# Optimization experiments

Hardware: AMD Instinct MI355X
Metric: run time of the kernel (lower is better)

## Reference

```python
import jax, jax.numpy as jnp
import numpy as np

B, L, D = 8, 2048, 256
DH = 256.0


def setup_inputs() -> dict:
    key = jax.random.key(0)
    ks = jax.random.split(key, 6)
    s = lambda k, shp: jax.random.normal(k, shp, dtype=jnp.float32)
    return {
        "inputQ": s(ks[0], (B, L, D)),
        "inputK": s(ks[1], (B, L, D)),
        "inputV": s(ks[2], (B, L, D)),
        "Wq": s(ks[3], (D, D)) * 0.05,
        "Wk": s(ks[4], (D, D)) * 0.05,
        "Wv": s(ks[5], (D, D)) * 0.05,
    }


def _skew(qe):
    # qe: [B, L, L] -> pad one zero column at front of last axis,
    # reshape [B, L+1, L], drop first row -> Srel [B, L, L]
    b, l, _ = qe.shape
    cat = jnp.concatenate([jnp.zeros((b, l, 1), qe.dtype), qe], axis=2)  # [B,L,L+1]
    reshaped = cat.reshape(b, l + 1, l)
    return reshaped[:, 1:, :]


def reference(inputQ, inputK, inputV, Wq, Wk, Wv):
    Q = jnp.einsum("bld,de->ble", inputQ, Wq)
    K = jnp.einsum("bld,de->ble", inputK, Wk)
    V = jnp.einsum("bld,de->ble", inputV, Wv)
    E = K - Q                                   # [B,L,D]
    QE = jnp.einsum("bqd,bkd->bqk", Q, E)       # Q @ E^T
    Srel = _skew(QE)
    QKt = jnp.einsum("bqd,bkd->bqk", Q, K)
    attn = jax.nn.softmax((QKt + Srel) / jnp.sqrt(jnp.float32(DH)), axis=-1)
    return jnp.einsum("bqk,bkd->bqd", attn, V)
```

## Files before the change

### kernel.cpp

```cpp
#include <hip/hip_runtime.h>
#include <hip/hip_fp16.h>
#include <stdint.h>

typedef _Float16 f16;
typedef _Float16 f16x2 __attribute__((ext_vector_type(2)));
typedef _Float16 f16x4 __attribute__((ext_vector_type(4)));
typedef _Float16 f16x8 __attribute__((ext_vector_type(8)));
typedef __fp16 fp16x2 __attribute__((ext_vector_type(2)));
typedef float f32x4 __attribute__((ext_vector_type(4)));

#define NB 8
#define NL 2048
#define ND 256
#define QKV_ELEMS (NB * NL * ND)

__device__ __forceinline__ f32x4 mfma16(f16x8 a, f16x8 b, f32x4 c) {
  return __builtin_amdgcn_mfma_f32_16x16x32_f16(a, b, c, 0, 0, 0);
}

__global__ void k0_wt(const float* __restrict__ Wq, const float* __restrict__ Wk,
                      const float* __restrict__ Wv, f16* __restrict__ WT) {
  int id = blockIdx.x * 256 + threadIdx.x;
  int m = id >> 16;
  int r = id & 65535;
  int k = r >> 8, n = r & 255;
  const float* W = (m == 0) ? Wq : (m == 1) ? Wk : Wv;
  WT[m * 65536 + n * 256 + k] = (f16)W[k * 256 + n];
}

__global__ __launch_bounds__(256) void k1_proj(
    const float* __restrict__ Aq, const float* __restrict__ Ak, const float* __restrict__ Av,
    const f16* __restrict__ WT, f16* __restrict__ Qh, f16* __restrict__ Kh,
    f16* __restrict__ Vh) {
  const int m = blockIdx.y;
  const float* A = (m == 0) ? Aq : (m == 1) ? Ak : Av;
  f16* O = (m == 0) ? Qh : (m == 1) ? Kh : Vh;
  const f16* Wm = WT + m * 65536;
  const int row0 = blockIdx.x * 64;
  const int tid = threadIdx.x;
  const int lane = tid & 63, w = tid >> 6;

  __shared__ f16 Ald[64 * 64];
  __shared__ f16 Wld[256 * 64];

  f32x4 acc[16];
#pragma unroll
  for (int i = 0; i < 16; ++i) acc[i] = f32x4{0.f, 0.f, 0.f, 0.f};

  for (int kb = 0; kb < 4; ++kb) {
    __syncthreads();
    {
      const int r = tid >> 2, c0 = (tid & 3) * 16;
      const float* src = A + (size_t)(row0 + r) * ND + kb * 64 + c0;
      f16x8 h0, h1;
#pragma unroll
      for (int j = 0; j < 8; ++j) h0[j] = (f16)src[j];
#pragma unroll
      for (int j = 0; j < 8; ++j) h1[j] = (f16)src[8 + j];
      const int sw = (r & 7) << 4;
      *(f16x8*)((char*)Ald + r * 128 + ((c0 * 2) ^ sw)) = h0;
      *(f16x8*)((char*)Ald + r * 128 + ((c0 * 2 + 16) ^ sw)) = h1;
    }
    {
      const int n = tid;
      const f16* src = Wm + n * 256 + kb * 64;
      const int sw = (n & 7) << 4;
#pragma unroll
      for (int j = 0; j < 8; ++j) {
        f16x8 v = *(const f16x8*)(src + j * 8);
        *(f16x8*)((char*)Wld + n * 128 + ((j * 16) ^ sw)) = v;
      }
    }
    __syncthreads();
#pragma unroll
    for (int kk = 0; kk < 2; ++kk) {
      const int arow = w * 16 + (lane & 15);
      const int ko = kk * 64 + (lane >> 4) * 16;
      f16x8 a = *(const f16x8*)((char*)Ald + arow * 128 + (ko ^ ((arow & 7) << 4)));
#pragma unroll
      for (int nt = 0; nt < 16; ++nt) {
        const int n = nt * 16 + (lane & 15);
        f16x8 b = *(const f16x8*)((char*)Wld + n * 128 + (ko ^ ((n & 7) << 4)));
        acc[nt] = mfma16(a, b, acc[nt]);
      }
    }
  }
  const int rl = (lane >> 4) * 4;
#pragma unroll
  for (int nt = 0; nt < 16; ++nt) {
    const int col = nt * 16 + (lane & 15);
#pragma unroll
    for (int j = 0; j < 4; ++j)
      O[(size_t)(row0 + w * 16 + rl + j) * ND + col] = (f16)acc[nt][j];
  }
}

__global__ __launch_bounds__(256) void k2_qe(const f16* __restrict__ Qh,
                                             const f16* __restrict__ Kh,
                                             f16* __restrict__ QEh) {
  const int b = blockIdx.z;
  const int m0 = blockIdx.x * 128, n0 = blockIdx.y * 128;
  const int tid = threadIdx.x, lane = tid & 63, w = tid >> 6;
  const int wr = (w >> 1) * 64, wc = (w & 1) * 64;
  const f16* Qb = Qh + (size_t)b * NL * ND;
  const f16* Kb = Kh + (size_t)b * NL * ND;

  __shared__ f16 As[128 * 64];
  __shared__ f16 Bs[128 * 64];

  f32x4 acc[4][4];
#pragma unroll
  for (int i = 0; i < 4; ++i)
#pragma unroll
    for (int j = 0; j < 4; ++j) acc[i][j] = f32x4{0.f, 0.f, 0.f, 0.f};

  for (int kb = 0; kb < 4; ++kb) {
    __syncthreads();
#pragma unroll
    for (int j = 0; j < 4; ++j) {
      const int c = j * 256 + tid;
      const int r = c >> 3;
      const int ko = (c & 7) * 16;
      const int sw = (r & 7) << 4;
      f16x8 va = *(const f16x8*)((const char*)(Qb + (size_t)(m0 + r) * ND + kb * 64) + ko);
      *(f16x8*)((char*)As + r * 128 + (ko ^ sw)) = va;
      f16x8 vk = *(const f16x8*)((const char*)(Kb + (size_t)(n0 + r) * ND + kb * 64) + ko);
      f16x8 vq = *(const f16x8*)((const char*)(Qb + (size_t)(n0 + r) * ND + kb * 64) + ko);
      *(f16x8*)((char*)Bs + r * 128 + (ko ^ sw)) = vk - vq;
    }
    __syncthreads();
#pragma unroll
    for (int kk = 0; kk < 2; ++kk) {
      const int ko = kk * 64 + (lane >> 4) * 16;
      f16x8 a[4], bf[4];
#pragma unroll
      for (int mt = 0; mt < 4; ++mt) {
        const int r = wr + mt * 16 + (lane & 15);
        a[mt] = *(const f16x8*)((char*)As + r * 128 + (ko ^ ((r & 7) << 4)));
      }
#pragma unroll
      for (int nt = 0; nt < 4; ++nt) {
        const int r = wc + nt * 16 + (lane & 15);
        bf[nt] = *(const f16x8*)((char*)Bs + r * 128 + (ko ^ ((r & 7) << 4)));
      }
#pragma unroll
      for (int mt = 0; mt < 4; ++mt)
#pragma unroll
        for (int nt = 0; nt < 4; ++nt) acc[mt][nt] = mfma16(a[mt], bf[nt], acc[mt][nt]);
    }
  }
  f16* outb = QEh + (size_t)b * NL * NL;
#pragma unroll
  for (int mt = 0; mt < 4; ++mt)
#pragma unroll
    for (int nt = 0; nt < 4; ++nt) {
      const int col = n0 + wc + nt * 16 + (lane & 15);
#pragma unroll
      for (int j = 0; j < 4; ++j) {
        const int row = m0 + wr + mt * 16 + (lane >> 4) * 4 + j;
        outb[(size_t)row * NL + col] = (f16)acc[mt][nt][j];
      }
    }
}

#define KVBUF 36864
#define NITP 16
__global__ __launch_bounds__(256, 2) void k3_part(
    const f16* __restrict__ Qh, const f16* __restrict__ Kh, const f16* __restrict__ Vh,
    const f16* __restrict__ QEh, f16* __restrict__ Pac, float* __restrict__ Pml) {
  __shared__ char smem[KVBUF];
  const int b = blockIdx.y;
  const int g = blockIdx.z;
  const int q0 = blockIdx.x * 64;
  const int tid = threadIdx.x, lane = tid & 63, w = tid >> 6;
  const int qw = q0 + w * 16;
  const int gi = lane >> 4;

  const f16* Qb = Qh + (size_t)b * NL * ND;
  const f16* Kb = Kh + (size_t)b * NL * ND;
  const f16* Vb = Vh + (size_t)b * NL * ND;
  const f16* QEb = QEh + (size_t)b * NL * NL;

  f16x8 qf[8];
  {
    const int r = qw + (lane & 15);
#pragma unroll
    for (int kk = 0; kk < 8; ++kk)
      qf[kk] = *(const f16x8*)(Qb + (size_t)r * ND + kk * 32 + gi * 8);
  }

  f32x4 acc[16];
#pragma unroll
  for (int i = 0; i < 16; ++i) acc[i] = f32x4{0.f, 0.f, 0.f, 0.f};
  float mrun = -1e30f, lrun = 0.f;

  f16x8 kst[4], vst[4];
  const int kp = tid & 15, dch = tid >> 4;

  auto stage_load = [&](int t) {
    const f16* Ks = Kb + (size_t)(g * NITP + t) * 32 * ND;
#pragma unroll
    for (int j = 0; j < 4; ++j) {
      const int c = j * 256 + tid;
      kst[j] = *(const f16x8*)(Ks + (c >> 5) * ND + (c & 31) * 8);
    }
    const f16* Vs = Vb + (size_t)(g * NITP + t) * 32 * ND;
    vst[0] = *(const f16x8*)(Vs + (2 * kp) * ND + dch * 16);
    vst[1] = *(const f16x8*)(Vs + (2 * kp) * ND + dch * 16 + 8);
    vst[2] = *(const f16x8*)(Vs + (2 * kp + 1) * ND + dch * 16);
    vst[3] = *(const f16x8*)(Vs + (2 * kp + 1) * ND + dch * 16 + 8);
  };
  auto stage_write = [&]() {
    char* Kld = smem;
    char* Vld = smem + 16384;
#pragma unroll
    for (int j = 0; j < 4; ++j) {
      const int c = j * 256 + tid;
      const int key = c >> 5, d0 = (c & 31) * 16;
      *(f16x8*)(Kld + key * 512 + (d0 ^ ((key & 7) << 4))) = kst[j];
    }
#pragma unroll
    for (int jj = 0; jj < 16; ++jj) {
      f16x2 pr;
      pr.x = (jj < 8) ? vst[0][jj & 7] : vst[1][jj & 7];
      pr.y = (jj < 8) ? vst[2][jj & 7] : vst[3][jj & 7];
      *(f16x2*)(Vld + (dch * 16 + jj) * 80 + kp * 4) = pr;
    }
  };

  stage_load(0);
  stage_write();
  __syncthreads();

  const int qa = qw + (lane & 15);

  for (int t = 0; t < NITP; ++t) {
    const int k0 = (g * NITP + t) * 32;

    float srel[2][4];
#pragma unroll
    for (int nt = 0; nt < 2; ++nt)
#pragma unroll
      for (int j = 0; j < 4; ++j) {
        const int k = k0 + nt * 16 + gi * 4 + j;
        const int dq = k - qa;
        const size_t a1 = (size_t)qa * NL + (size_t)(NL - 1 + dq);
        const size_t a2 = (size_t)(qa + 1) * NL + (size_t)(dq - 2);
        const float v = (float)QEb[(dq <= 0) ? a1 : a2];
        srel[nt][j] = (dq == 1) ? 0.f : v;
      }

    if (t < NITP - 1) stage_load(t + 1);

    const char* Kld = smem;
    const char* Vld = smem + 16384;

    f32x4 s[2] = {f32x4{0.f, 0.f, 0.f, 0.f}, f32x4{0.f, 0.f, 0.f, 0.f}};
#pragma unroll
    for (int kk = 0; kk < 8; ++kk) {
      const int ko = kk * 64 + gi * 16;
#pragma unroll
      for (int nt = 0; nt < 2; ++nt) {
        const int key = nt * 16 + (lane & 15);
        f16x8 af = *(const f16x8*)(Kld + key * 512 + (ko ^ ((key & 7) << 4)));
        s[nt] = mfma16(af, qf[kk], s[nt]);
      }
    }

    float sv[2][4];
#pragma unroll
    for (int nt = 0; nt < 2; ++nt)
#pragma unroll
      for (int j = 0; j < 4; ++j) sv[nt][j] = 0.0625f * (s[nt][j] + srel[nt][j]);

    float pm = fmaxf(fmaxf(fmaxf(sv[0][0], sv[0][1]), fmaxf(sv[0][2], sv[0][3])),
                     fmaxf(fmaxf(sv[1][0], sv[1][1]), fmaxf(sv[1][2], sv[1][3])));
    pm = fmaxf(pm, __shfl_xor(pm, 16, 64));
    pm = fmaxf(pm, __shfl_xor(pm, 32, 64));

    float p[2][4];
    if (__any(pm > mrun + 8.f)) {
      const float mn = fmaxf(mrun, pm);
      const float al = __expf(mrun - mn);
      mrun = mn;
#pragma unroll
      for (int nt = 0; nt < 2; ++nt)
#pragma unroll
        for (int j = 0; j < 4; ++j) p[nt][j] = __expf(sv[nt][j] - mrun);
      float rs = (p[0][0] + p[0][1]) + (p[0][2] + p[0][3]) +
                 (p[1][0] + p[1][1]) + (p[1][2] + p[1][3]);
      rs += __shfl_xor(rs, 16, 64);
      rs += __shfl_xor(rs, 32, 64);
      lrun = lrun * al + rs;
#pragma unroll
      for (int j = 0; j < 4; ++j) {
        const float aj = __shfl(al, gi * 4 + j, 16);
#pragma unroll
        for (int dt = 0; dt < 16; ++dt) acc[dt][j] *= aj;
      }
    } else {
#pragma unroll
      for (int nt = 0; nt < 2; ++nt)
#pragma unroll
        for (int j = 0; j < 4; ++j) p[nt][j] = __expf(sv[nt][j] - mrun);
      float rs = (p[0][0] + p[0][1]) + (p[0][2] + p[0][3]) +
                 (p[1][0] + p[1][1]) + (p[1][2] + p[1][3]);
      rs += __shfl_xor(rs, 16, 64);
      rs += __shfl_xor(rs, 32, 64);
      lrun += rs;
    }

    union {
      fp16x2 h2[2];
      f16x4 h4;
    } pu0, pu1;
    pu0.h2[0] = __builtin_amdgcn_cvt_pkrtz(p[0][0], p[0][1]);
    pu0.h2[1] = __builtin_amdgcn_cvt_pkrtz(p[0][2], p[0][3]);
    pu1.h2[0] = __builtin_amdgcn_cvt_pkrtz(p[1][0], p[1][1]);
    pu1.h2[1] = __builtin_amdgcn_cvt_pkrtz(p[1][2], p[1][3]);

#pragma unroll
    for (int dt = 0; dt < 16; ++dt) {
      const char* vrow = Vld + (dt * 16 + (lane & 15)) * 80 + 8 * gi;
      f16x4 v0 = *(const f16x4*)(vrow);
      f16x4 v1 = *(const f16x4*)(vrow + 32);
      acc[dt] = __builtin_amdgcn_mfma_f32_16x16x16f16(pu0.h4, v0, acc[dt], 0, 0, 0);
      acc[dt] = __builtin_amdgcn_mfma_f32_16x16x16f16(pu1.h4, v1, acc[dt], 0, 0, 0);
    }

    __syncthreads();
    if (t < NITP - 1) stage_write();
    __syncthreads();
  }

  const float inv = 1.f / lrun;
  f16* Pb = Pac + ((size_t)g * (NB * NL) + (size_t)b * NL) * ND;
#pragma unroll
  for (int j = 0; j < 4; ++j) {
    const float invj = __shfl(inv, gi * 4 + j, 16);
    const int row = qw + gi * 4 + j;
#pragma unroll
    for (int dt = 0; dt < 16; ++dt)
      Pb[(size_t)row * ND + dt * 16 + (lane & 15)] = (f16)(acc[dt][j] * invj);
  }
  if (lane < 16) {
    const size_t r = (size_t)g * (NB * NL) + (size_t)b * NL + qw + lane;
    Pml[r * 2 + 0] = mrun;
    Pml[r * 2 + 1] = lrun;
  }
}

__global__ __launch_bounds__(256) void k4_comb(const f16* __restrict__ Pac,
                                               const float* __restrict__ Pml,
                                               float* __restrict__ Out) {
  const int row = blockIdx.x * 4 + (threadIdx.x >> 6);
  const int lane = threadIdx.x & 63;
  float m[4], l[4];
#pragma unroll
  for (int gq = 0; gq < 4; ++gq) {
    const size_t r = (size_t)gq * (NB * NL) + row;
    m[gq] = Pml[r * 2 + 0];
    l[gq] = Pml[r * 2 + 1];
  }
  const float M = fmaxf(fmaxf(m[0], m[1]), fmaxf(m[2], m[3]));
  float wgt[4];
  float denom = 0.f;
#pragma unroll
  for (int gq = 0; gq < 4; ++gq) {
    wgt[gq] = l[gq] * __expf(m[gq] - M);
    denom += wgt[gq];
  }
  const float inv = 1.f / denom;
  const size_t base = (size_t)row * ND + lane * 4;
  float o[4] = {0.f, 0.f, 0.f, 0.f};
#pragma unroll
  for (int gq = 0; gq < 4; ++gq) {
    f16x4 p = *(const f16x4*)(Pac + (size_t)gq * (NB * NL) * ND + base);
    const float s = wgt[gq] * inv;
#pragma unroll
    for (int e = 0; e < 4; ++e) o[e] += (float)p[e] * s;
  }
  f32x4 ov = {o[0], o[1], o[2], o[3]};
  *(f32x4*)(Out + base) = ov;
}

#define NIT 32
__global__ __launch_bounds__(512, 2) void k3_attn(
    const f16* __restrict__ Qh, const f16* __restrict__ Kh, const f16* __restrict__ Vh,
    const f16* __restrict__ QEh, float* __restrict__ Out) {
  extern __shared__ char smemd[];
  const int b = blockIdx.y;
  const int q0 = blockIdx.x * 64;
  const int tid = threadIdx.x, lane = tid & 63, w = tid >> 6;
  const int g = w >> 2, wq = w & 3;
  const int qw = q0 + wq * 16;
  const int lt = tid & 255;
  const int gi = lane >> 4;

  float* Cst = (float*)smemd;
  float* ml = (float*)(smemd + 65536);

  const f16* Qb = Qh + (size_t)b * NL * ND;
  const f16* Kb = Kh + (size_t)b * NL * ND;
  const f16* Vb = Vh + (size_t)b * NL * ND;
  const f16* QEb = QEh + (size_t)b * NL * NL;

  f16x8 qf[8];
  {
    const int r = qw + (lane & 15);
#pragma unroll
    for (int kk = 0; kk < 8; ++kk)
      qf[kk] = *(const f16x8*)(Qb + (size_t)r * ND + kk * 32 + gi * 8);
  }

  f32x4 acc[16];
#pragma unroll
  for (int i = 0; i < 16; ++i) acc[i] = f32x4{0.f, 0.f, 0.f, 0.f};
  float mrun = -1e30f, lrun = 0.f;

  f16x8 kst[4], vst[4];
  const int kp = lt & 15, dch = lt >> 4;

  auto stage_load = [&](int t) {
    const f16* Ks = Kb + (size_t)(g * NIT + t) * 32 * ND;
#pragma unroll
    for (int j = 0; j < 4; ++j) {
      const int c = j * 256 + lt;
      kst[j] = *(const f16x8*)(Ks + (c >> 5) * ND + (c & 31) * 8);
    }
    const f16* Vs = Vb + (size_t)(g * NIT + t) * 32 * ND;
    vst[0] = *(const f16x8*)(Vs + (2 * kp) * ND + dch * 16);
    vst[1] = *(const f16x8*)(Vs + (2 * kp) * ND + dch * 16 + 8);
    vst[2] = *(const f16x8*)(Vs + (2 * kp + 1) * ND + dch * 16);
    vst[3] = *(const f16x8*)(Vs + (2 * kp + 1) * ND + dch * 16 + 8);
  };
  auto stage_write = [&]() {
    char* Kld = smemd + g * KVBUF;
    char* Vld = Kld + 16384;
#pragma unroll
    for (int j = 0; j < 4; ++j) {
      const int c = j * 256 + lt;
      const int key = c >> 5, d0 = (c & 31) * 16;
      *(f16x8*)(Kld + key * 512 + (d0 ^ ((key & 7) << 4))) = kst[j];
    }
#pragma unroll
    for (int jj = 0; jj < 16; ++jj) {
      f16x2 pr;
      pr.x = (jj < 8) ? vst[0][jj & 7] : vst[1][jj & 7];
      pr.y = (jj < 8) ? vst[2][jj & 7] : vst[3][jj & 7];
      *(f16x2*)(Vld + (dch * 16 + jj) * 80 + kp * 4) = pr;
    }
  };

  stage_load(0);
  stage_write();
  __syncthreads();

  const int qa = qw + (lane & 15);

  for (int t = 0; t < NIT; ++t) {
    const int k0 = (g * NIT + t) * 32;

    float srel[2][4];
#pragma unroll
    for (int nt = 0; nt < 2; ++nt)
#pragma unroll
      for (int j = 0; j < 4; ++j) {
        const int k = k0 + nt * 16 + gi * 4 + j;
        const int dq = k - qa;
        const size_t a1 = (size_t)qa * NL + (size_t)(NL - 1 + dq);
        const size_t a2 = (size_t)(qa + 1) * NL + (size_t)(dq - 2);
        const float v = (float)QEb[(dq <= 0) ? a1 : a2];
        srel[nt][j] = (dq == 1) ? 0.f : v;
      }

    if (t < NIT - 1) stage_load(t + 1);

    const char* Kld = smemd + g * KVBUF;
    const char* Vld = Kld + 16384;

    f32x4 s[2] = {f32x4{0.f, 0.f, 0.f, 0.f}, f32x4{0.f, 0.f, 0.f, 0.f}};
#pragma unroll
    for (int kk = 0; kk < 8; ++kk) {
      const int ko = kk * 64 + gi * 16;
#pragma unroll
      for (int nt = 0; nt < 2; ++nt) {
        const int key = nt * 16 + (lane & 15);
        f16x8 af = *(const f16x8*)(Kld + key * 512 + (ko ^ ((key & 7) << 4)));
        s[nt] = mfma16(af, qf[kk], s[nt]);
      }
    }

    float sv[2][4];
#pragma unroll
    for (int nt = 0; nt < 2; ++nt)
#pragma unroll
      for (int j = 0; j < 4; ++j) sv[nt][j] = 0.0625f * (s[nt][j] + srel[nt][j]);

    float pm = fmaxf(fmaxf(fmaxf(sv[0][0], sv[0][1]), fmaxf(sv[0][2], sv[0][3])),
                     fmaxf(fmaxf(sv[1][0], sv[1][1]), fmaxf(sv[1][2], sv[1][3])));
    pm = fmaxf(pm, __shfl_xor(pm, 16, 64));
    pm = fmaxf(pm, __shfl_xor(pm, 32, 64));

    float p[2][4];
    if (__any(pm > mrun + 8.f)) {
      const float mn = fmaxf(mrun, pm);
      const float al = __expf(mrun - mn);
      mrun = mn;
#pragma unroll
      for (int nt = 0; nt < 2; ++nt)
#pragma unroll
        for (int j = 0; j < 4; ++j) p[nt][j] = __expf(sv[nt][j] - mrun);
      float rs = (p[0][0] + p[0][1]) + (p[0][2] + p[0][3]) +
                 (p[1][0] + p[1][1]) + (p[1][2] + p[1][3]);
      rs += __shfl_xor(rs, 16, 64);
      rs += __shfl_xor(rs, 32, 64);
      lrun = lrun * al + rs;
#pragma unroll
      for (int j = 0; j < 4; ++j) {
        const float aj = __shfl(al, gi * 4 + j, 16);
#pragma unroll
        for (int dt = 0; dt < 16; ++dt) acc[dt][j] *= aj;
      }
    } else {
#pragma unroll
      for (int nt = 0; nt < 2; ++nt)
#pragma unroll
        for (int j = 0; j < 4; ++j) p[nt][j] = __expf(sv[nt][j] - mrun);
      float rs = (p[0][0] + p[0][1]) + (p[0][2] + p[0][3]) +
                 (p[1][0] + p[1][1]) + (p[1][2] + p[1][3]);
      rs += __shfl_xor(rs, 16, 64);
      rs += __shfl_xor(rs, 32, 64);
      lrun += rs;
    }

    union {
      fp16x2 h2[2];
      f16x4 h4;
    } pu0, pu1;
    pu0.h2[0] = __builtin_amdgcn_cvt_pkrtz(p[0][0], p[0][1]);
    pu0.h2[1] = __builtin_amdgcn_cvt_pkrtz(p[0][2], p[0][3]);
    pu1.h2[0] = __builtin_amdgcn_cvt_pkrtz(p[1][0], p[1][1]);
    pu1.h2[1] = __builtin_amdgcn_cvt_pkrtz(p[1][2], p[1][3]);

#pragma unroll
    for (int dt = 0; dt < 16; ++dt) {
      const char* vrow = Vld + (dt * 16 + (lane & 15)) * 80 + 8 * gi;
      f16x4 v0 = *(const f16x4*)(vrow);
      f16x4 v1 = *(const f16x4*)(vrow + 32);
      acc[dt] = __builtin_amdgcn_mfma_f32_16x16x16f16(pu0.h4, v0, acc[dt], 0, 0, 0);
      acc[dt] = __builtin_amdgcn_mfma_f32_16x16x16f16(pu1.h4, v1, acc[dt], 0, 0, 0);
    }

    __syncthreads();
    if (t < NIT - 1) stage_write();
    __syncthreads();
  }

  if (g == 1) {
#pragma unroll
    for (int dt = 0; dt < 16; ++dt)
#pragma unroll
      for (int j = 0; j < 4; ++j)
        Cst[wq * 4096 + (gi * 4 + j) * 256 + dt * 16 + (lane & 15)] = acc[dt][j];
    if (lane < 16) {
      ml[(wq * 16 + lane) * 2 + 0] = mrun;
      ml[(wq * 16 + lane) * 2 + 1] = lrun;
    }
  }
  __syncthreads();
  if (g == 0) {
    float* Ob = Out + (size_t)b * NL * ND;
#pragma unroll
    for (int j = 0; j < 4; ++j) {
      const int rloc = gi * 4 + j;
      const float m0r = __shfl(mrun, rloc, 16);
      const float l0r = __shfl(lrun, rloc, 16);
      const float m1 = ml[(wq * 16 + rloc) * 2 + 0];
      const float l1 = ml[(wq * 16 + rloc) * 2 + 1];
      const float M = fmaxf(m0r, m1);
      const float c0 = __expf(m0r - M), c1 = __expf(m1 - M);
      const float inv = 1.f / (l0r * c0 + l1 * c1);
      const int row = qw + rloc;
#pragma unroll
      for (int dt = 0; dt < 16; ++dt) {
        const float o1 = Cst[wq * 4096 + rloc * 256 + dt * 16 + (lane & 15)];
        Ob[(size_t)row * ND + dt * 16 + (lane & 15)] = (acc[dt][j] * c0 + o1 * c1) * inv;
      }
    }
  }
}

extern "C" void kernel_launch(void* const* d_in, const int* in_sizes, int n_in,
                              void* d_out, int out_size, void* d_ws, size_t ws_size,
                              hipStream_t stream) {
  (void)in_sizes; (void)n_in; (void)out_size;
  const float* inQ = (const float*)d_in[0];
  const float* inK = (const float*)d_in[1];
  const float* inV = (const float*)d_in[2];
  const float* Wq = (const float*)d_in[3];
  const float* Wk = (const float*)d_in[4];
  const float* Wv = (const float*)d_in[5];
  float* out = (float*)d_out;

  f16* ws = (f16*)d_ws;
  f16* Qh = ws;
  f16* Kh = Qh + (size_t)QKV_ELEMS;
  f16* Vh = Kh + (size_t)QKV_ELEMS;
  f16* WT = Vh + (size_t)QKV_ELEMS;
  f16* QEh = WT + 3 * 65536;
  f16* Pac = QEh + (size_t)NB * NL * NL;
  float* Pml = (float*)(Pac + (size_t)4 * QKV_ELEMS);
  const size_t need = (size_t)((char*)(Pml + 4 * NB * NL * 2) - (char*)d_ws);

  k0_wt<<<dim3(768), dim3(256), 0, stream>>>(Wq, Wk, Wv, WT);
  k1_proj<<<dim3(256, 3), dim3(256), 0, stream>>>(inQ, inK, inV, WT, Qh, Kh, Vh);
  k2_qe<<<dim3(16, 16, 8), dim3(256), 0, stream>>>(Qh, Kh, QEh);
  if (ws_size >= need) {
    k3_part<<<dim3(32, 8, 4), dim3(256), 0, stream>>>(Qh, Kh, Vh, QEh, Pac, Pml);
    k4_comb<<<dim3(NB * NL / 4), dim3(256), 0, stream>>>(Pac, Pml, out);
  } else {
    k3_attn<<<dim3(32, 8), dim3(512), 73728, stream>>>(Qh, Kh, Vh, QEh, out);
  }
}
```

Before: 189.9 us.

## Split PV by head-dim across waves, pretranspose V, async-copy K to LDS

Adds a kernel that transposes V into a d-major layout so each wave loads its own V fragments straight from global memory. The P@V work is repartitioned: each wave covers a 64-wide slice of the head dimension for all 64 queries, with P tiles and rescale factors exchanged through shared memory. K tiles are double-buffered in LDS with global_load_lds, which removes the register staging and one barrier per iteration. The cost is an extra transpose pass, more workspace, and LDS traffic for sharing P, and the new path runs only when the workspace is large enough.

```diff
diff --git a/kernel.cpp b/kernel.cpp
--- a/kernel.cpp
+++ b/kernel.cpp
@@ -16,6 +16,12 @@
 
 __device__ __forceinline__ f32x4 mfma16(f16x8 a, f16x8 b, f32x4 c) {
   return __builtin_amdgcn_mfma_f32_16x16x32_f16(a, b, c, 0, 0, 0);
+}
+
+__device__ __forceinline__ void gl_lds16(const void* g, void* l) {
+  __builtin_amdgcn_global_load_lds(
+      (const __attribute__((address_space(1))) void*)g,
+      (__attribute__((address_space(3))) void*)l, 16, 0, 0);
 }
 
 __global__ void k0_wt(const float* __restrict__ Wq, const float* __restrict__ Wk,
@@ -95,6 +101,33 @@
   }
 }
 
+__global__ __launch_bounds__(256) void k1c_vt(const f16* __restrict__ Vh,
+                                              f16* __restrict__ VT) {
+  const int b = blockIdx.z;
+  const int k0 = blockIdx.x * 64;
+  const int d0 = blockIdx.y * 64;
+  __shared__ f16 T[64][72];
+  const int tid = threadIdx.x;
+  const f16* Vb = Vh + (size_t)b * NL * ND;
+  {
+    const int r = tid >> 2, c = (tid & 3) * 16;
+    f16x8 a = *(const f16x8*)(Vb + (size_t)(k0 + r) * ND + d0 + c);
+    f16x8 bq = *(const f16x8*)(Vb + (size_t)(k0 + r) * ND + d0 + c + 8);
+    *(f16x8*)&T[r][c] = a;
+    *(f16x8*)&T[r][c + 8] = bq;
+  }
+  __syncthreads();
+  {
+    const int d = tid >> 2, c = (tid & 3) * 16;
+    f16 tmp[16];
+#pragma unroll
+    for (int j = 0; j < 16; ++j) tmp[j] = T[c + j][d];
+    f16* dst = VT + (size_t)b * ND * NL + (size_t)(d0 + d) * NL + k0 + c;
+    *(f16x8*)dst = *(f16x8*)&tmp[0];
+    *(f16x8*)(dst + 8) = *(f16x8*)&tmp[8];
+  }
+}
+
 __global__ __launch_bounds__(256) void k2_qe(const f16* __restrict__ Qh,
                                              const f16* __restrict__ Kh,
                                              f16* __restrict__ QEh) {
@@ -163,78 +196,55 @@
     }
 }
 
-#define KVBUF 36864
 #define NITP 16
 __global__ __launch_bounds__(256, 2) void k3_part(
-    const f16* __restrict__ Qh, const f16* __restrict__ Kh, const f16* __restrict__ Vh,
+    const f16* __restrict__ Qh, const f16* __restrict__ Kh, const f16* __restrict__ VT,
     const f16* __restrict__ QEh, f16* __restrict__ Pac, float* __restrict__ Pml) {
-  __shared__ char smem[KVBUF];
-  const int b = blockIdx.y;
-  const int g = blockIdx.z;
-  const int q0 = blockIdx.x * 64;
-  const int tid = threadIdx.x, lane = tid & 63, w = tid >> 6;
+  __shared__ char Kld[2][16384];
+  __shared__ char Pfr[2][4096];
+  __shared__ float alf[2][64];
+  __shared__ int rfl[2][4];
+  __shared__ float mlinv[64];
+
+  const int b = blockIdx.y, g = blockIdx.z, q0 = blockIdx.x * 64;
+  const int tid = threadIdx.x, lane = tid & 63, w = tid >> 6, gi = lane >> 4;
   const int qw = q0 + w * 16;
-  const int gi = lane >> 4;
+  const int dbase = w * 64;
 
   const f16* Qb = Qh + (size_t)b * NL * ND;
   const f16* Kb = Kh + (size_t)b * NL * ND;
-  const f16* Vb = Vh + (size_t)b * NL * ND;
+  const f16* VTb = VT + (size_t)b * ND * NL;
   const f16* QEb = QEh + (size_t)b * NL * NL;
 
+  const int qa = qw + (lane & 15);
   f16x8 qf[8];
-  {
-    const int r = qw + (lane & 15);
-#pragma unroll
-    for (int kk = 0; kk < 8; ++kk)
-      qf[kk] = *(const f16x8*)(Qb + (size_t)r * ND + kk * 32 + gi * 8);
-  }
-
-  f32x4 acc[16];
-#pragma unroll
-  for (int i = 0; i < 16; ++i) acc[i] = f32x4{0.f, 0.f, 0.f, 0.f};
+#pragma unroll
+  for (int kk = 0; kk < 8; ++kk)
+    qf[kk] = *(const f16x8*)(Qb + (size_t)qa * ND + kk * 32 + gi * 8);
+
+  f32x4 acc[4][4];
+#pragma unroll
+  for (int i = 0; i < 4; ++i)
+#pragma unroll
+    for (int j = 0; j < 4; ++j) acc[i][j] = f32x4{0.f, 0.f, 0.f, 0.f};
   float mrun = -1e30f, lrun = 0.f;
 
-  f16x8 kst[4], vst[4];
-  const int kp = tid & 15, dch = tid >> 4;
-
-  auto stage_load = [&](int t) {
-    const f16* Ks = Kb + (size_t)(g * NITP + t) * 32 * ND;
-#pragma unroll
-    for (int j = 0; j < 4; ++j) {
-      const int c = j * 256 + tid;
-      kst[j] = *(const f16x8*)(Ks + (c >> 5) * ND + (c & 31) * 8);
-    }
-    const f16* Vs = Vb + (size_t)(g * NITP + t) * 32 * ND;
-    vst[0] = *(const f16x8*)(Vs + (2 * kp) * ND + dch * 16);
-    vst[1] = *(const f16x8*)(Vs + (2 * kp) * ND + dch * 16 + 8);
-    vst[2] = *(const f16x8*)(Vs + (2 * kp + 1) * ND + dch * 16);
-    vst[3] = *(const f16x8*)(Vs + (2 * kp + 1) * ND + dch * 16 + 8);
+  auto kstage = [&](int t, int buf) {
+    const char* src = (const char*)(Kb + (size_t)(g * NITP + t) * 32 * ND);
+#pragma unroll
+    for (int i = 0; i < 4; ++i) {
+      const int chunk = w * 4 + i;
+      const int r = chunk * 2 + (lane >> 5);
+      const int co = ((lane & 31) * 16) ^ ((r & 7) << 4);
+      gl_lds16(src + r * 512 + co, Kld[buf] + chunk * 1024);
+    }
   };
-  auto stage_write = [&]() {
-    char* Kld = smem;
-    char* Vld = smem + 16384;
-#pragma unroll
-    for (int j = 0; j < 4; ++j) {
-      const int c = j * 256 + tid;
-      const int key = c >> 5, d0 = (c & 31) * 16;
-      *(f16x8*)(Kld + key * 512 + (d0 ^ ((key & 7) << 4))) = kst[j];
-    }
-#pragma unroll
-    for (int jj = 0; jj < 16; ++jj) {
-      f16x2 pr;
-      pr.x = (jj < 8) ? vst[0][jj & 7] : vst[1][jj & 7];
-      pr.y = (jj < 8) ? vst[2][jj & 7] : vst[3][jj & 7];
-      *(f16x2*)(Vld + (dch * 16 + jj) * 80 + kp * 4) = pr;
-    }
-  };
-
-  stage_load(0);
-  stage_write();
+
+  kstage(0, 0);
   __syncthreads();
 
-  const int qa = qw + (lane & 15);
-
   for (int t = 0; t < NITP; ++t) {
+    const int pb = t & 1;
     const int k0 = (g * NITP + t) * 32;
 
     float srel[2][4];
@@ -250,10 +260,7 @@
         srel[nt][j] = (dq == 1) ? 0.f : v;
       }
 
-    if (t < NITP - 1) stage_load(t + 1);
-
-    const char* Kld = smem;
-    const char* Vld = smem + 16384;
+    if (t < NITP - 1) kstage(t + 1, pb ^ 1);
 
     f32x4 s[2] = {f32x4{0.f, 0.f, 0.f, 0.f}, f32x4{0.f, 0.f, 0.f, 0.f}};
 #pragma unroll
@@ -262,7 +269,7 @@
 #pragma unroll
       for (int nt = 0; nt < 2; ++nt) {
         const int key = nt * 16 + (lane & 15);
-        f16x8 af = *(const f16x8*)(Kld + key * 512 + (ko ^ ((key & 7) << 4)));
+        f16x8 af = *(const f16x8*)(Kld[pb] + key * 512 + (ko ^ ((key & 7) << 4)));
         s[nt] = mfma16(af, qf[kk], s[nt]);
       }
     }
@@ -278,37 +285,26 @@
     pm = fmaxf(pm, __shfl_xor(pm, 16, 64));
     pm = fmaxf(pm, __shfl_xor(pm, 32, 64));
 
+    const int doresc = (int)__any(pm > mrun + 8.f);
+    if (lane == 0) rfl[pb][w] = doresc;
+
     float p[2][4];
-    if (__any(pm > mrun + 8.f)) {
+    float al = 1.f;
+    if (doresc) {
       const float mn = fmaxf(mrun, pm);
-      const float al = __expf(mrun - mn);
+      al = __expf(mrun - mn);
       mrun = mn;
-#pragma unroll
-      for (int nt = 0; nt < 2; ++nt)
-#pragma unroll
-        for (int j = 0; j < 4; ++j) p[nt][j] = __expf(sv[nt][j] - mrun);
-      float rs = (p[0][0] + p[0][1]) + (p[0][2] + p[0][3]) +
-                 (p[1][0] + p[1][1]) + (p[1][2] + p[1][3]);
-      rs += __shfl_xor(rs, 16, 64);
-      rs += __shfl_xor(rs, 32, 64);
-      lrun = lrun * al + rs;
-#pragma unroll
-      for (int j = 0; j < 4; ++j) {
-        const float aj = __shfl(al, gi * 4 + j, 16);
-#pragma unroll
-        for (int dt = 0; dt < 16; ++dt) acc[dt][j] *= aj;
-      }
-    } else {
-#pragma unroll
-      for (int nt = 0; nt < 2; ++nt)
-#pragma unroll
-        for (int j = 0; j < 4; ++j) p[nt][j] = __expf(sv[nt][j] - mrun);
-      float rs = (p[0][0] + p[0][1]) + (p[0][2] + p[0][3]) +
-                 (p[1][0] + p[1][1]) + (p[1][2] + p[1][3]);
-      rs += __shfl_xor(rs, 16, 64);
-      rs += __shfl_xor(rs, 32, 64);
-      lrun += rs;
-    }
+    }
+#pragma unroll
+    for (int nt = 0; nt < 2; ++nt)
+#pragma unroll
+      for (int j = 0; j < 4; ++j) p[nt][j] = __expf(sv[nt][j] - mrun);
+    float rs = (p[0][0] + p[0][1]) + (p[0][2] + p[0][3]) +
+               (p[1][0] + p[1][1]) + (p[1][2] + p[1][3]);
+    rs += __shfl_xor(rs, 16, 64);
+    rs += __shfl_xor(rs, 32, 64);
+    lrun = lrun * al + rs;
+    if (gi == 0) alf[pb][w * 16 + (lane & 15)] = al;
 
     union {
       fp16x2 h2[2];
@@ -318,36 +314,60 @@
     pu0.h2[1] = __builtin_amdgcn_cvt_pkrtz(p[0][2], p[0][3]);
     pu1.h2[0] = __builtin_amdgcn_cvt_pkrtz(p[1][0], p[1][1]);
     pu1.h2[1] = __builtin_amdgcn_cvt_pkrtz(p[1][2], p[1][3]);
-
-#pragma unroll
-    for (int dt = 0; dt < 16; ++dt) {
-      const char* vrow = Vld + (dt * 16 + (lane & 15)) * 80 + 8 * gi;
-      f16x4 v0 = *(const f16x4*)(vrow);
-      f16x4 v1 = *(const f16x4*)(vrow + 32);
-      acc[dt] = __builtin_amdgcn_mfma_f32_16x16x16f16(pu0.h4, v0, acc[dt], 0, 0, 0);
-      acc[dt] = __builtin_amdgcn_mfma_f32_16x16x16f16(pu1.h4, v1, acc[dt], 0, 0, 0);
-    }
+    *(f16x4*)(Pfr[pb] + (w * 2 + 0) * 512 + lane * 8) = pu0.h4;
+    *(f16x4*)(Pfr[pb] + (w * 2 + 1) * 512 + lane * 8) = pu1.h4;
+
+    f16x4 vf[4][2];
+#pragma unroll
+    for (int dt = 0; dt < 4; ++dt)
+#pragma unroll
+      for (int nt = 0; nt < 2; ++nt)
+        vf[dt][nt] = *(const f16x4*)(VTb + (size_t)(dbase + dt * 16 + (lane & 15)) * NL +
+                                     k0 + nt * 16 + 4 * gi);
 
     __syncthreads();
-    if (t < NITP - 1) stage_write();
-    __syncthreads();
-  }
-
-  const float inv = 1.f / lrun;
-  f16* Pb = Pac + ((size_t)g * (NB * NL) + (size_t)b * NL) * ND;
-#pragma unroll
-  for (int j = 0; j < 4; ++j) {
-    const float invj = __shfl(inv, gi * 4 + j, 16);
-    const int row = qw + gi * 4 + j;
-#pragma unroll
-    for (int dt = 0; dt < 16; ++dt)
-      Pb[(size_t)row * ND + dt * 16 + (lane & 15)] = (f16)(acc[dt][j] * invj);
-  }
+
+    if (rfl[pb][0] | rfl[pb][1] | rfl[pb][2] | rfl[pb][3]) {
+#pragma unroll
+      for (int qt = 0; qt < 4; ++qt)
+#pragma unroll
+        for (int j = 0; j < 4; ++j) {
+          const float a = alf[pb][qt * 16 + 4 * gi + j];
+#pragma unroll
+          for (int dt = 0; dt < 4; ++dt) acc[qt][dt][j] *= a;
+        }
+    }
+
+#pragma unroll
+    for (int qt = 0; qt < 4; ++qt) {
+      f16x4 pa0 = *(const f16x4*)(Pfr[pb] + (qt * 2 + 0) * 512 + lane * 8);
+      f16x4 pa1 = *(const f16x4*)(Pfr[pb] + (qt * 2 + 1) * 512 + lane * 8);
+#pragma unroll
+      for (int dt = 0; dt < 4; ++dt) {
+        acc[qt][dt] = __builtin_amdgcn_mfma_f32_16x16x16f16(pa0, vf[dt][0], acc[qt][dt], 0, 0, 0);
+        acc[qt][dt] = __builtin_amdgcn_mfma_f32_16x16x16f16(pa1, vf[dt][1], acc[qt][dt], 0, 0, 0);
+      }
+    }
+  }
+
+  if (gi == 0) mlinv[w * 16 + (lane & 15)] = 1.f / lrun;
   if (lane < 16) {
     const size_t r = (size_t)g * (NB * NL) + (size_t)b * NL + qw + lane;
     Pml[r * 2 + 0] = mrun;
     Pml[r * 2 + 1] = lrun;
   }
+  __syncthreads();
+  f16* Pb = Pac + ((size_t)g * (NB * NL) + (size_t)b * NL + q0) * ND;
+#pragma unroll
+  for (int qt = 0; qt < 4; ++qt)
+#pragma unroll
+    for (int j = 0; j < 4; ++j) {
+      const int row = qt * 16 + 4 * gi + j;
+      const float iv = mlinv[row];
+#pragma unroll
+      for (int dt = 0; dt < 4; ++dt)
+        Pb[(size_t)row * ND + dbase + dt * 16 + (lane & 15)] = (f16)(acc[qt][dt][j] * iv);
+    }
 }
 
 __global__ __launch_bounds__(256) void k4_comb(const f16* __restrict__ Pac,
@@ -384,6 +404,7 @@
   *(f32x4*)(Out + base) = ov;
 }
 
+#define KVBUF 36864
 #define NIT 32
 __global__ __launch_bounds__(512, 2) void k3_attn(
     const f16* __restrict__ Qh, const f16* __restrict__ Kh, const f16* __restrict__ Vh,
@@ -611,13 +632,15 @@
   f16* QEh = WT + 3 * 65536;
   f16* Pac = QEh + (size_t)NB * NL * NL;
   float* Pml = (float*)(Pac + (size_t)4 * QKV_ELEMS);
-  const size_t need = (size_t)((char*)(Pml + 4 * NB * NL * 2) - (char*)d_ws);
+  f16* VT = (f16*)(Pml + 4 * NB * NL * 2);
+  const size_t need = (size_t)((char*)(VT + (size_t)QKV_ELEMS) - (char*)d_ws);
 
   k0_wt<<<dim3(768), dim3(256), 0, stream>>>(Wq, Wk, Wv, WT);
   k1_proj<<<dim3(256, 3), dim3(256), 0, stream>>>(inQ, inK, inV, WT, Qh, Kh, Vh);
   k2_qe<<<dim3(16, 16, 8), dim3(256), 0, stream>>>(Qh, Kh, QEh);
   if (ws_size >= need) {
-    k3_part<<<dim3(32, 8, 4), dim3(256), 0, stream>>>(Qh, Kh, Vh, QEh, Pac, Pml);
+    k1c_vt<<<dim3(32, 4, 8), dim3(256), 0, stream>>>(Vh, VT);
+    k3_part<<<dim3(32, 8, 4), dim3(256), 0, stream>>>(Qh, Kh, VT, QEh, Pac, Pml);
     k4_comb<<<dim3(NB * NL / 4), dim3(256), 0, stream>>>(Pac, Pml, out);
   } else {
     k3_attn<<<dim3(32, 8), dim3(512), 73728, stream>>>(Qh, Kh, Vh, QEh, out);
```

Result: slower. 208.4 us (+9.7%).
